# Kernel tuning notes

Hardware: AMD Instinct MI355X
Metric: run time of the kernel (lower is better)

The kernel has to match this reference:

```python
import jax, jax.numpy as jnp
import numpy as np

B, L, C, D = 4, 2048, 64, 4


def setup_inputs() -> dict:
    key = jax.random.key(0)
    k1, k2, k3, k4 = jax.random.split(key, 4)
    # |A| kept < ~0.92 so the length-2048 recurrence stays bounded
    A_re = jax.random.uniform(k1, (B, L, C, D), jnp.float32, -0.65, 0.65)
    A_im = jax.random.uniform(k2, (B, L, C, D), jnp.float32, -0.65, 0.65)
    X_re = jax.random.normal(k3, (B, L, C, D, D), jnp.float32)
    X_im = jax.random.normal(k4, (B, L, C, D, D), jnp.float32)
    return {"A_re": A_re, "A_im": A_im, "X_re": X_re, "X_im": X_im}


def _combine(c1, c2):
    # first-order linear recurrence combine: (a, x) o (b, y) = (b*a, b*x + y)
    a1, x1 = c1
    a2, x2 = c2
    return a2 * a1, a2 * x1 + x2


def reference(A_re, A_im, X_re, X_im):
    # Diagonal complex pscan: Y[t] = A[t] * Y[t-1] + X[t], elementwise,
    # with diagonal A [B,L,C,D] broadcast over the trailing D dim of X [B,L,C,D,D]
    A = (A_re + 1j * A_im).astype(jnp.complex64)[..., None]  # [B,L,C,D,1]
    X = (X_re + 1j * X_im).astype(jnp.complex64)             # [B,L,C,D,D]
    _, Y = jax.lax.associative_scan(_combine, (A, X), axis=1)
    # return real view [B,L,C,D,D,2] (real, imag) like torch.view_as_real
    return jnp.stack([Y.real, Y.imag], axis=-1)
```

## Files before the change

kernel.cpp:

```cpp
#include <hip/hip_runtime.h>

#define BB 4
#define LL 2048
#define CC 64
#define DD 4
#define NN (CC * DD * DD)
#define AN (CC * DD)
#define TPB 256
#define TT (LL / TPB)

typedef float f32x4 __attribute__((ext_vector_type(4)));

__global__ __launch_bounds__(256) void pscan_onepass(
    const float* __restrict__ A_re, const float* __restrict__ A_im,
    const f32x4* __restrict__ X_re4, const f32x4* __restrict__ X_im4,
    f32x4* __restrict__ out4) {
  const int sid = (blockIdx.x & 7) * 128 + (blockIdx.x >> 3);
  const int n4  = sid & (AN - 1);
  const int b   = sid >> 8;
  const int tid = threadIdx.x;
  const int t0  = tid * TT;
  const int base = (b * LL + t0) * AN + n4;

  float ar[TT], ai[TT];
  f32x4 xr[TT], xi[TT];
#pragma unroll
  for (int t = 0; t < TT; ++t) {
    ar[t] = A_re[base + t * AN];
    ai[t] = A_im[base + t * AN];
    xr[t] = X_re4[base + t * AN];
    xi[t] = X_im4[base + t * AN];
  }

  float p_re = 1.f, p_im = 0.f;
  float s_re[4] = {0.f, 0.f, 0.f, 0.f};
  float s_im[4] = {0.f, 0.f, 0.f, 0.f};
#pragma unroll
  for (int t = 0; t < TT; ++t) {
    const float are = ar[t], aim = ai[t];
    const float npre = are * p_re - aim * p_im;
    const float npim = are * p_im + aim * p_re;
    p_re = npre; p_im = npim;
#pragma unroll
    for (int j = 0; j < 4; ++j) {
      const float nsre = are * s_re[j] - aim * s_im[j] + xr[t][j];
      const float nsim = are * s_im[j] + aim * s_re[j] + xi[t][j];
      s_re[j] = nsre; s_im[j] = nsim;
    }
  }

  __shared__ float lds[TPB][11];
  lds[tid][0] = p_re; lds[tid][1] = p_im;
#pragma unroll
  for (int j = 0; j < 4; ++j) { lds[tid][2 + j] = s_re[j]; lds[tid][6 + j] = s_im[j]; }

  float vp_re = p_re, vp_im = p_im;
  float vs_re[4], vs_im[4];
#pragma unroll
  for (int j = 0; j < 4; ++j) { vs_re[j] = s_re[j]; vs_im[j] = s_im[j]; }

  for (int d = 1; d < TPB; d <<= 1) {
    __syncthreads();
    float wp_re = 1.f, wp_im = 0.f;
    float ws_re[4] = {0.f, 0.f, 0.f, 0.f};
    float ws_im[4] = {0.f, 0.f, 0.f, 0.f};
    if (tid >= d) {
      wp_re = lds[tid - d][0]; wp_im = lds[tid - d][1];
#pragma unroll
      for (int j = 0; j < 4; ++j) { ws_re[j] = lds[tid - d][2 + j]; ws_im[j] = lds[tid - d][6 + j]; }
    }
    __syncthreads();
    if (tid >= d) {
      const float np_re = vp_re * wp_re - vp_im * wp_im;
      const float np_im = vp_re * wp_im + vp_im * wp_re;
#pragma unroll
      for (int j = 0; j < 4; ++j) {
        const float ns_re = vp_re * ws_re[j] - vp_im * ws_im[j] + vs_re[j];
        const float ns_im = vp_re * ws_im[j] + vp_im * ws_re[j] + vs_im[j];
        vs_re[j] = ns_re; vs_im[j] = ns_im;
      }
      vp_re = np_re; vp_im = np_im;
      lds[tid][0] = vp_re; lds[tid][1] = vp_im;
#pragma unroll
      for (int j = 0; j < 4; ++j) { lds[tid][2 + j] = vs_re[j]; lds[tid][6 + j] = vs_im[j]; }
    }
  }
  __syncthreads();

  float y_re[4] = {0.f, 0.f, 0.f, 0.f};
  float y_im[4] = {0.f, 0.f, 0.f, 0.f};
  if (tid > 0) {
#pragma unroll
    for (int j = 0; j < 4; ++j) { y_re[j] = lds[tid - 1][2 + j]; y_im[j] = lds[tid - 1][6 + j]; }
  }

  const int ob = (b * LL + t0) * (2 * AN) + n4 * 2;
#pragma unroll
  for (int t = 0; t < TT; ++t) {
    const float are = ar[t], aim = ai[t];
#pragma unroll
    for (int j = 0; j < 4; ++j) {
      const float ny_re = are * y_re[j] - aim * y_im[j] + xr[t][j];
      const float ny_im = are * y_im[j] + aim * y_re[j] + xi[t][j];
      y_re[j] = ny_re; y_im[j] = ny_im;
    }
    f32x4 o0 = {y_re[0], y_im[0], y_re[1], y_im[1]};
    f32x4 o1 = {y_re[2], y_im[2], y_re[3], y_im[3]};
    out4[ob + t * (2 * AN)]     = o0;
    out4[ob + t * (2 * AN) + 1] = o1;
  }
}

extern "C" void kernel_launch(void* const* d_in, const int* in_sizes, int n_in,
                              void* d_out, int out_size, void* d_ws, size_t ws_size,
                              hipStream_t stream) {
  const float* A_re  = (const float*)d_in[0];
  const float* A_im  = (const float*)d_in[1];
  const f32x4* X_re4 = (const f32x4*)d_in[2];
  const f32x4* X_im4 = (const f32x4*)d_in[3];
  f32x4* out4 = (f32x4*)d_out;
  (void)d_ws; (void)ws_size;

  const int blocks = BB * AN;
  pscan_onepass<<<blocks, TPB, 0, stream>>>(A_re, A_im, X_re4, X_im4, out4);
}
```

Measured before the change: 173.1 us.

## Process four adjacent channels per block with 512-thread segmented scan and X reload

Each block now handles four adjacent n4 channels with 128 time segments of 16 steps, instead of one channel with 256 segments of 8. Adjacent lanes read contiguous A and X elements, which coalesces global loads and stores into wider transactions; the per-block remap that interleaved blocks is dropped. X is no longer held in registers but reloaded during the output pass, trading a second global (likely cached) read for lower register pressure. The longer sequential chunks add serial latency per thread, while the LDS scan needs fewer steps.

Result: faster. 167.9 us (-3.0%).

```diff
diff --git a/kernel.cpp b/kernel.cpp
--- a/kernel.cpp
+++ b/kernel.cpp
@@ -6,71 +6,72 @@
 #define DD 4
 #define NN (CC * DD * DD)
 #define AN (CC * DD)
-#define TPB 256
-#define TT (LL / TPB)
+#define TPB 512
+#define N4PB 4
+#define NSEGS (TPB / N4PB)
+#define TT (LL / NSEGS)
 
 typedef float f32x4 __attribute__((ext_vector_type(4)));
 
-__global__ __launch_bounds__(256) void pscan_onepass(
+__global__ __launch_bounds__(512) void pscan_onepass2(
     const float* __restrict__ A_re, const float* __restrict__ A_im,
     const f32x4* __restrict__ X_re4, const f32x4* __restrict__ X_im4,
     f32x4* __restrict__ out4) {
-  const int sid = (blockIdx.x & 7) * 128 + (blockIdx.x >> 3);
-  const int n4  = sid & (AN - 1);
-  const int b   = sid >> 8;
-  const int tid = threadIdx.x;
-  const int t0  = tid * TT;
+  const int b    = blockIdx.x >> 6;
+  const int n4g  = blockIdx.x & 63;
+  const int tid  = threadIdx.x;
+  const int n4l  = tid & (N4PB - 1);
+  const int tseg = tid >> 2;
+  const int n4   = n4g * N4PB + n4l;
+  const int t0   = tseg * TT;
   const int base = (b * LL + t0) * AN + n4;
 
   float ar[TT], ai[TT];
-  f32x4 xr[TT], xi[TT];
-#pragma unroll
-  for (int t = 0; t < TT; ++t) {
-    ar[t] = A_re[base + t * AN];
-    ai[t] = A_im[base + t * AN];
-    xr[t] = X_re4[base + t * AN];
-    xi[t] = X_im4[base + t * AN];
-  }
-
   float p_re = 1.f, p_im = 0.f;
   float s_re[4] = {0.f, 0.f, 0.f, 0.f};
   float s_im[4] = {0.f, 0.f, 0.f, 0.f};
 #pragma unroll
   for (int t = 0; t < TT; ++t) {
-    const float are = ar[t], aim = ai[t];
+    const float are = A_re[base + t * AN];
+    const float aim = A_im[base + t * AN];
+    ar[t] = are; ai[t] = aim;
+    const f32x4 xr = X_re4[base + t * AN];
+    const f32x4 xi = X_im4[base + t * AN];
     const float npre = are * p_re - aim * p_im;
     const float npim = are * p_im + aim * p_re;
     p_re = npre; p_im = npim;
 #pragma unroll
     for (int j = 0; j < 4; ++j) {
-      const float nsre = are * s_re[j] - aim * s_im[j] + xr[t][j];
-      const float nsim = are * s_im[j] + aim * s_re[j] + xi[t][j];
+      const float nsre = are * s_re[j] - aim * s_im[j] + xr[j];
+      const float nsim = are * s_im[j] + aim * s_re[j] + xi[j];
       s_re[j] = nsre; s_im[j] = nsim;
     }
   }
 
-  __shared__ float lds[TPB][11];
-  lds[tid][0] = p_re; lds[tid][1] = p_im;
+  __shared__ float lds[TPB * 11];
+  const int q = tid * 11;
+  lds[q + 0] = p_re; lds[q + 1] = p_im;
 #pragma unroll
-  for (int j = 0; j < 4; ++j) { lds[tid][2 + j] = s_re[j]; lds[tid][6 + j] = s_im[j]; }
+  for (int j = 0; j < 4; ++j) { lds[q + 2 + j] = s_re[j]; lds[q + 6 + j] = s_im[j]; }
 
   float vp_re = p_re, vp_im = p_im;
   float vs_re[4], vs_im[4];
 #pragma unroll
   for (int j = 0; j < 4; ++j) { vs_re[j] = s_re[j]; vs_im[j] = s_im[j]; }
 
-  for (int d = 1; d < TPB; d <<= 1) {
+  for (int d = 1; d < NSEGS; d <<= 1) {
     __syncthreads();
     float wp_re = 1.f, wp_im = 0.f;
     float ws_re[4] = {0.f, 0.f, 0.f, 0.f};
     float ws_im[4] = {0.f, 0.f, 0.f, 0.f};
-    if (tid >= d) {
-      wp_re = lds[tid - d][0]; wp_im = lds[tid - d][1];
+    if (tseg >= d) {
+      const int q2 = q - d * (N4PB * 11);
+      wp_re = lds[q2 + 0]; wp_im = lds[q2 + 1];
 #pragma unroll
-      for (int j = 0; j < 4; ++j) { ws_re[j] = lds[tid - d][2 + j]; ws_im[j] = lds[tid - d][6 + j]; }
+      for (int j = 0; j < 4; ++j) { ws_re[j] = lds[q2 + 2 + j]; ws_im[j] = lds[q2 + 6 + j]; }
     }
     __syncthreads();
-    if (tid >= d) {
+    if (tseg >= d) {
       const float np_re = vp_re * wp_re - vp_im * wp_im;
       const float np_im = vp_re * wp_im + vp_im * wp_re;
 #pragma unroll
@@ -80,28 +81,31 @@
         vs_re[j] = ns_re; vs_im[j] = ns_im;
       }
       vp_re = np_re; vp_im = np_im;
-      lds[tid][0] = vp_re; lds[tid][1] = vp_im;
+      lds[q + 0] = vp_re; lds[q + 1] = vp_im;
 #pragma unroll
-      for (int j = 0; j < 4; ++j) { lds[tid][2 + j] = vs_re[j]; lds[tid][6 + j] = vs_im[j]; }
+      for (int j = 0; j < 4; ++j) { lds[q + 2 + j] = vs_re[j]; lds[q + 6 + j] = vs_im[j]; }
     }
   }
   __syncthreads();
 
   float y_re[4] = {0.f, 0.f, 0.f, 0.f};
   float y_im[4] = {0.f, 0.f, 0.f, 0.f};
-  if (tid > 0) {
+  if (tseg > 0) {
+    const int qc = q - N4PB * 11;
 #pragma unroll
-    for (int j = 0; j < 4; ++j) { y_re[j] = lds[tid - 1][2 + j]; y_im[j] = lds[tid - 1][6 + j]; }
+    for (int j = 0; j < 4; ++j) { y_re[j] = lds[qc + 2 + j]; y_im[j] = lds[qc + 6 + j]; }
   }
 
   const int ob = (b * LL + t0) * (2 * AN) + n4 * 2;
 #pragma unroll
   for (int t = 0; t < TT; ++t) {
     const float are = ar[t], aim = ai[t];
+    const f32x4 xr = X_re4[base + t * AN];
+    const f32x4 xi = X_im4[base + t * AN];
 #pragma unroll
     for (int j = 0; j < 4; ++j) {
-      const float ny_re = are * y_re[j] - aim * y_im[j] + xr[t][j];
-      const float ny_im = are * y_im[j] + aim * y_re[j] + xi[t][j];
+      const float ny_re = are * y_re[j] - aim * y_im[j] + xr[j];
+      const float ny_im = are * y_im[j] + aim * y_re[j] + xi[j];
       y_re[j] = ny_re; y_im[j] = ny_im;
     }
     f32x4 o0 = {y_re[0], y_im[0], y_re[1], y_im[1]};
@@ -121,6 +125,6 @@
   f32x4* out4 = (f32x4*)d_out;
   (void)d_ws; (void)ws_size;
 
-  const int blocks = BB * AN;
-  pscan_onepass<<<blocks, TPB, 0, stream>>>(A_re, A_im, X_re4, X_im4, out4);
+  const int blocks = BB * (AN / N4PB);
+  pscan_onepass2<<<blocks, TPB, 0, stream>>>(A_re, A_im, X_re4, X_im4, out4);
 }
```
